# Kernel optimization log

Measured on AMD Instinct MI355X. Metric: run time of the kernel, lower is better.

Reference implementation:

```python
import jax, jax.numpy as jnp
import numpy as np

C = 1024   # hidden_size
H = 16     # num_heads
D = C // H # head dim
M = 4096   # mlp hidden
T = 1024   # motion seq len
B = 8      # batch
TA = 1024  # audio seq len


def _w(key, shape):
    return jax.random.normal(key, shape, dtype=jnp.float32) * 0.02


def setup_inputs() -> dict:
    key = jax.random.key(0)
    ks = jax.random.split(key, 32)
    inp = {
        'x': jax.random.normal(ks[0], (T, B, C), dtype=jnp.float32),
        'c': jax.random.normal(ks[1], (B, C), dtype=jnp.float32),
        'padding_mask': jax.random.randint(ks[2], (B, T), 0, 2, dtype=jnp.int32),
        'audio_seq': jax.random.normal(ks[3], (TA, B, C), dtype=jnp.float32),
        'audio_mask': jax.random.randint(ks[4], (B, TA), 0, 2, dtype=jnp.int32),
        # adaLN modulation: SiLU -> Linear(C, 6C)
        'w_ada': _w(ks[5], (C, 6 * C)), 'b_ada': jnp.zeros((6 * C,), jnp.float32),
        # self-attention q/k/v/proj
        'wq': _w(ks[6], (C, C)), 'bq': jnp.zeros((C,), jnp.float32),
        'wk': _w(ks[7], (C, C)), 'bk': jnp.zeros((C,), jnp.float32),
        'wv': _w(ks[8], (C, C)), 'bv': jnp.zeros((C,), jnp.float32),
        'wo': _w(ks[9], (C, C)), 'bo': jnp.zeros((C,), jnp.float32),
        # cross-attention q/k/v/proj
        'cwq': _w(ks[10], (C, C)), 'cbq': jnp.zeros((C,), jnp.float32),
        'cwk': _w(ks[11], (C, C)), 'cbk': jnp.zeros((C,), jnp.float32),
        'cwv': _w(ks[12], (C, C)), 'cbv': jnp.zeros((C,), jnp.float32),
        'cwo': _w(ks[13], (C, C)), 'cbo': jnp.zeros((C,), jnp.float32),
        # MLP fc1/fc2
        'w1': _w(ks[14], (C, M)), 'b1': jnp.zeros((M,), jnp.float32),
        'w2': _w(ks[15], (M, C)), 'b2': jnp.zeros((C,), jnp.float32),
    }
    return inp


def _ln(x):
    # LayerNorm(elementwise_affine=False, eps=1e-6)
    mu = jnp.mean(x, axis=-1, keepdims=True)
    var = jnp.var(x, axis=-1, keepdims=True)
    return (x - mu) * jax.lax.rsqrt(var + 1e-6)


def _modulate(x, shift, scale):
    # batch-first x [B, T, C]; shift/scale [B, C]
    return x * (1.0 + scale[:, None, :]) + shift[:, None, :]


def _mha(xq, xkv, wq, bq, wk, bk, wv, bv, wo, bo, mask):
    # xq [B, Tq, C], xkv [B, Tk, C], mask [B, Tk] (nonzero = masked)
    b, tq, _ = xq.shape
    tk = xkv.shape[1]
    q = (xq @ wq + bq).reshape(b, tq, H, D)
    k = (xkv @ wk + bk).reshape(b, tk, H, D)
    v = (xkv @ wv + bv).reshape(b, tk, H, D)
    att = jnp.einsum('bqhd,bkhd->bhqk', q, k) * (1.0 / np.sqrt(D))
    att = jnp.where(mask[:, None, None, :] != 0, -jnp.inf, att)
    att = jax.nn.softmax(att, axis=-1)
    y = jnp.einsum('bhqk,bkhd->bqhd', att, v).reshape(b, tq, C)
    return y @ wo + bo


def _gelu_tanh(x):
    return jax.nn.gelu(x, approximate=True)


def reference(x, c, padding_mask, audio_seq, audio_mask,
              w_ada, b_ada, wq, bq, wk, bk, wv, bv, wo, bo,
              cwq, cbq, cwk, cbk, cwv, cbv, cwo, cbo,
              w1, b1, w2, b2):
    # adaLN modulation parameters
    mod = jax.nn.silu(c) @ w_ada + b_ada                 # [B, 6C]
    (shift_msa, scale_msa, gate_msa,
     shift_mlp, scale_mlp, gate_mlp) = jnp.split(mod, 6, axis=1)

    # x is sequence-first [T, B, C] (padding_mask batch dim matches x dim 1)
    x_batch = jnp.transpose(x, (1, 0, 2))                # [B, T, C]
    x_mod = _modulate(_ln(x_batch), shift_msa, scale_msa)
    attn_out = _mha(x_mod, x_mod, wq, bq, wk, bk, wv, bv, wo, bo, padding_mask)
    x = x + gate_msa[None, :, :] * jnp.transpose(attn_out, (1, 0, 2))

    # cross attention (reuses msa shift/scale/gate, as in the source)
    xb = jnp.transpose(x, (1, 0, 2))                     # [B, T, C]
    ab = jnp.transpose(audio_seq, (1, 0, 2))             # [B, TA, C]
    x_cross_in = _modulate(_ln(xb), shift_msa, scale_msa)
    cross_out = _mha(x_cross_in, ab, cwq, cbq, cwk, cbk, cwv, cbv, cwo, cbo,
                     audio_mask)
    x = x + gate_msa[None, :, :] * jnp.transpose(cross_out, (1, 0, 2))

    # MLP
    xb = jnp.transpose(x, (1, 0, 2))
    h = _modulate(_ln(xb), shift_mlp, scale_mlp)
    mlp_out = _gelu_tanh(h @ w1 + b1) @ w2 + b2
    x = x + gate_mlp[None, :, :] * jnp.transpose(mlp_out, (1, 0, 2))
    return x
```

## Files before the change

### kernel.cpp

```cpp
#include <hip/hip_runtime.h>
#include <math.h>

#define T_SEQ 1024
#define TA_SEQ 1024
#define BATCH 8
#define CH 1024
#define NH 16
#define HD 64
#define MH 4096

typedef unsigned short u16;
typedef unsigned short u16x4 __attribute__((ext_vector_type(4)));
typedef unsigned short u16x8 __attribute__((ext_vector_type(8)));
typedef __bf16 bf16x8 __attribute__((ext_vector_type(8)));
typedef float f32x4 __attribute__((ext_vector_type(4)));

__device__ __forceinline__ u16 f2bf(float f) {
  unsigned int u = __builtin_bit_cast(unsigned int, f);
  u += 0x7FFFu + ((u >> 16) & 1u);
  return (u16)(u >> 16);
}
__device__ __forceinline__ u16 f2bf_trunc(float f) {
  return (u16)(__builtin_bit_cast(unsigned int, f) >> 16);
}
__device__ __forceinline__ bf16x8 ldbf8(const u16* p) {
  return __builtin_bit_cast(bf16x8, *reinterpret_cast<const u16x8*>(p));
}
__device__ __forceinline__ void gload_lds16(const u16* g, u16* l) {
  __builtin_amdgcn_global_load_lds(
      (const __attribute__((address_space(1))) unsigned int*)g,
      (__attribute__((address_space(3))) unsigned int*)l, 16, 0, 0);
}

#define ASM_BAR()   asm volatile("s_barrier" ::: "memory")
#define ASM_VM8()   asm volatile("s_waitcnt vmcnt(8)" ::: "memory")
#define ASM_VM6()   asm volatile("s_waitcnt vmcnt(6)" ::: "memory")
#define ASM_VM4()   asm volatile("s_waitcnt vmcnt(4)" ::: "memory")
#define ASM_VM3()   asm volatile("s_waitcnt vmcnt(3)" ::: "memory")
#define ASM_VM0()   asm volatile("s_waitcnt vmcnt(0)" ::: "memory")
#define ASM_LGKM0() asm volatile("s_waitcnt lgkmcnt(0)" ::: "memory")

__global__ void k_transpose_w(const float* __restrict__ in, u16* __restrict__ out,
                              int K, int N) {
  __shared__ float tile[32][33];
  int n0 = blockIdx.x * 32, k0 = blockIdx.y * 32;
  int tx = threadIdx.x, ty = threadIdx.y;
#pragma unroll
  for (int i = 0; i < 4; i++)
    tile[ty + i * 8][tx] = in[(size_t)(k0 + ty + i * 8) * N + n0 + tx];
  __syncthreads();
#pragma unroll
  for (int i = 0; i < 4; i++)
    out[(size_t)(n0 + ty + i * 8) * K + k0 + tx] = f2bf(tile[tx][ty + i * 8]);
}

struct P8f { const float* p[8]; };
struct P8u { u16* p[8]; };
__global__ void k_transpose8(P8f in8, P8u out8) {
  const float* __restrict__ in = in8.p[blockIdx.z];
  u16* __restrict__ out = out8.p[blockIdx.z];
  __shared__ float tile[32][33];
  int n0 = blockIdx.x * 32, k0 = blockIdx.y * 32;
  int tx = threadIdx.x, ty = threadIdx.y;
#pragma unroll
  for (int i = 0; i < 4; i++)
    tile[ty + i * 8][tx] = in[(size_t)(k0 + ty + i * 8) * CH + n0 + tx];
  __syncthreads();
#pragma unroll
  for (int i = 0; i < 4; i++)
    out[(size_t)(n0 + ty + i * 8) * CH + k0 + tx] = f2bf(tile[tx][ty + i * 8]);
}

__global__ void k_ada(const float* __restrict__ c, const float* __restrict__ w_ada,
                      const float* __restrict__ b_ada, float* __restrict__ mod) {
  __shared__ float sc[CH];
  int b = blockIdx.y;
  int tid = threadIdx.x;
  for (int i = tid; i < CH; i += 256) {
    float cv = c[b * CH + i];
    sc[i] = cv / (1.0f + expf(-cv));
  }
  __syncthreads();
  int n = blockIdx.x * 256 + tid;
  float acc = 0.0f;
  for (int k = 0; k < CH; k++) acc += sc[k] * w_ada[(size_t)k * (6 * CH) + n];
  mod[(size_t)b * (6 * CH) + n] = acc + b_ada[n];
}

__global__ void k_tbc_to_btc_bf16(const float* __restrict__ in, u16* __restrict__ out) {
  size_t i = (size_t)blockIdx.x * 256 + threadIdx.x;
  int c = (int)(i & (CH - 1));
  size_t tb = i >> 10;
  int b = (int)(tb & (BATCH - 1));
  size_t t = tb >> 3;
  out[((size_t)b * TA_SEQ + t) * CH + c] = f2bf(in[i]);
}

template <int IN_TBC>
__global__ void k_ln_mod(const float* __restrict__ src, const float* __restrict__ mod,
                         u16* __restrict__ out, float* __restrict__ xb_out,
                         int shift_sel, int scale_sel) {
  int row = blockIdx.x;
  int b = row >> 10;
  int tid = threadIdx.x;
  const float* xr;
  if (IN_TBC) {
    int t = row & (T_SEQ - 1);
    xr = src + ((size_t)t * BATCH + b) * CH;
  } else {
    xr = src + (size_t)row * CH;
  }
  float4 v = reinterpret_cast<const float4*>(xr)[tid];
  float s = v.x + v.y + v.z + v.w;
  float s2 = v.x * v.x + v.y * v.y + v.z * v.z + v.w * v.w;
#pragma unroll
  for (int off = 32; off > 0; off >>= 1) {
    s += __shfl_down(s, off);
    s2 += __shfl_down(s2, off);
  }
  __shared__ float red[8];
  __shared__ float stats[2];
  int wid = tid >> 6;
  if ((tid & 63) == 0) { red[wid] = s; red[4 + wid] = s2; }
  __syncthreads();
  if (tid == 0) {
    float a = red[0] + red[1] + red[2] + red[3];
    float a2 = red[4] + red[5] + red[6] + red[7];
    float mu = a * (1.0f / CH);
    float var = a2 * (1.0f / CH) - mu * mu;
    stats[0] = mu;
    stats[1] = rsqrtf(var + 1e-6f);
  }
  __syncthreads();
  float mu = stats[0], rs = stats[1];
  int c0 = tid * 4;
  if (IN_TBC)
    reinterpret_cast<float4*>(xb_out + (size_t)row * CH)[tid] = v;
  const float* sh = mod + (size_t)b * (6 * CH) + (size_t)shift_sel * CH + c0;
  const float* scl = mod + (size_t)b * (6 * CH) + (size_t)scale_sel * CH + c0;
  float xs[4] = {v.x, v.y, v.z, v.w};
  u16x4 o;
#pragma unroll
  for (int j = 0; j < 4; j++)
    o[j] = f2bf((xs[j] - mu) * rs * (1.0f + scl[j]) + sh[j]);
  *reinterpret_cast<u16x4*>(out + (size_t)row * CH + c0) = o;
}

__device__ __forceinline__ void mfma_quad(const bf16x8 (&af)[4], const bf16x8 (&bfr)[4],
                                          f32x4 (*arow)[4]) {
#pragma unroll
  for (int mi = 0; mi < 4; mi++)
#pragma unroll
    for (int ni = 0; ni < 4; ni++)
      arow[mi][ni] = __builtin_amdgcn_mfma_f32_16x16x32_bf16(af[mi], bfr[ni],
                                                             arow[mi][ni], 0, 0, 0);
}

__device__ __forceinline__ void gemm256_core(
    const u16* __restrict__ A, const u16* __restrict__ Bt, int K,
    int m0, int n0, int tid, u16* AS, u16* BS, f32x4 (&acc)[8][4]) {
  int wid = tid >> 6, lane = tid & 63;
  int wr = wid >> 2, wc = wid & 3;
  int lrow = lane & 15, quad = lane >> 4;
  int sx = (quad ^ ((lrow >> 1) & 3)) * 8;
  int aRow = wr * 128 + lrow;
  int bRow = wc * 64 + lrow;
  int rA = tid >> 2;
  int qsw = (((tid & 3) ^ ((tid >> 3) & 3)) << 3);
  const u16* gA = A + (size_t)(m0 + rA) * K + qsw;
  const u16* gB = Bt + (size_t)(n0 + rA) * K + qsw;
  const size_t r128 = (size_t)128 * K;
  u16* dA = AS + tid * 8;
  u16* dB = BS + tid * 8;
  const int NT = K >> 6;

#define STGA(dd, hh, tt) do { const u16* s_ = gA + ((tt) * 64 + (hh) * 32); \
    u16* d_ = dA + ((dd) * 2 + (hh)) * 8192; \
    gload_lds16(s_, d_); gload_lds16(s_ + r128, d_ + 4096); } while (0)
#define STGB(dd, hh, tt) do { const u16* s_ = gB + ((tt) * 64 + (hh) * 32); \
    u16* d_ = dB + ((dd) * 2 + (hh)) * 8192; \
    gload_lds16(s_, d_); gload_lds16(s_ + r128, d_ + 4096); } while (0)
#define RD_A(dd, kk, mh) do { const u16* b_ = AS + ((dd) * 2 + (kk)) * 8192; \
    int r_ = aRow + (mh) * 64; \
    af[0] = ldbf8(&b_[(r_) * 32 + sx]); \
    af[1] = ldbf8(&b_[(r_ + 16) * 32 + sx]); \
    af[2] = ldbf8(&b_[(r_ + 32) * 32 + sx]); \
    af[3] = ldbf8(&b_[(r_ + 48) * 32 + sx]); } while (0)
#define RD_B(dd, kk) do { const u16* b_ = BS + ((dd) * 2 + (kk)) * 8192; \
    bfr[0] = ldbf8(&b_[(bRow) * 32 + sx]); \
    bfr[1] = ldbf8(&b_[(bRow + 16) * 32 + sx]); \
    bfr[2] = ldbf8(&b_[(bRow + 32) * 32 + sx]); \
    bfr[3] = ldbf8(&b_[(bRow + 48) * 32 + sx]); } while (0)
#define PHASE_TAIL(mh) do { ASM_LGKM0(); __builtin_amdgcn_sched_barrier(0); \
    __builtin_amdgcn_s_setprio(1); mfma_quad(af, bfr, acc + (mh) * 4); \
    __builtin_amdgcn_s_setprio(0); ASM_BAR(); } while (0)

  STGA(0, 0, 0); STGB(0, 0, 0); STGA(0, 1, 0); STGB(0, 1, 0);
  STGA(1, 0, 1); STGB(1, 0, 1);
  ASM_VM8(); ASM_BAR();

  bf16x8 af[4], bfr[4];
  for (int t = 0; t < NT; ++t) {
    int d = t & 1;
    RD_A(d, 0, 0); RD_B(d, 0);
    if (t + 1 < NT) STGA(d ^ 1, 1, t + 1);
    PHASE_TAIL(0);
    RD_A(d, 0, 1);
    if (t + 1 < NT) STGB(d ^ 1, 1, t + 1);
    if (t == NT - 1) { ASM_VM0(); } else { ASM_VM8(); }
    PHASE_TAIL(1);
    RD_A(d, 1, 0); RD_B(d, 1);
    if (t + 2 < NT) STGA(d, 0, t + 2);
    PHASE_TAIL(0);
    RD_A(d, 1, 1);
    if (t + 2 < NT) STGB(d, 0, t + 2);
    if (t < NT - 2) { ASM_VM8(); } else if (t == NT - 2) { ASM_VM4(); }
    PHASE_TAIL(1);
  }
#undef STGA
#undef STGB
#undef RD_A
#undef RD_B
#undef PHASE_TAIL
}

template <int EPI>
__global__ __launch_bounds__(512, 2) void k_gemm256(
    const u16* __restrict__ A, const u16* __restrict__ Bt,
    const float* __restrict__ bias, u16* __restrict__ out_bf,
    float* __restrict__ xb, const float* __restrict__ mod, int gate_sel,
    int M, int N, int K) {
  __shared__ u16 AS[2 * 2 * 8192];
  __shared__ u16 BS[2 * 2 * 8192];
  int m0 = blockIdx.x * 256, n0 = blockIdx.y * 256;
  int tid = threadIdx.x;
  int wid = tid >> 6, lane = tid & 63;
  int wr = wid >> 2, wc = wid & 3;
  int lrow = lane & 15, quad = lane >> 4;
  f32x4 acc[8][4];
#pragma unroll
  for (int mi = 0; mi < 8; mi++)
#pragma unroll
    for (int ni = 0; ni < 4; ni++) acc[mi][ni] = {0.f, 0.f, 0.f, 0.f};
  gemm256_core(A, Bt, K, m0, n0, tid, AS, BS, acc);
#pragma unroll
  for (int mi = 0; mi < 8; mi++)
#pragma unroll
    for (int ni = 0; ni < 4; ni++) {
      int col = n0 + wc * 64 + ni * 16 + lrow;
      float bval = bias[col];
#pragma unroll
      for (int r = 0; r < 4; r++) {
        int row = m0 + wr * 128 + mi * 16 + quad * 4 + r;
        float v = acc[mi][ni][r] + bval;
        if (EPI == 1) {
          int b = row >> 10;
          float g = mod[(size_t)b * (6 * CH) + (size_t)gate_sel * CH + col];
          xb[(size_t)row * N + col] += g * v;
        } else if (EPI == 2) {
          float t2 = 2.3021181302f * (v + 0.044715f * v * v * v);
          float gel = v * __builtin_amdgcn_rcpf(1.0f + exp2f(-t2));
          out_bf[(size_t)row * N + col] = f2bf(gel);
        } else {
          out_bf[(size_t)row * N + col] = f2bf(v * 0.18033688011112042f);
        }
      }
    }
}

__global__ __launch_bounds__(512, 2) void k_qkv256(
    const u16* __restrict__ A, const u16* __restrict__ Bt,
    const float* __restrict__ bq, const float* __restrict__ bk,
    const float* __restrict__ bv,
    u16* __restrict__ qout, u16* __restrict__ kout, u16* __restrict__ vt) {
  __shared__ u16 AS[2 * 2 * 8192];
  __shared__ u16 BS[2 * 2 * 8192];
  int m0 = blockIdx.x * 256, n0 = blockIdx.y * 256;
  int tid = threadIdx.x;
  int wid = tid >> 6, lane = tid & 63;
  int wr = wid >> 2, wc = wid & 3;
  int lrow = lane & 15, quad = lane >> 4;
  f32x4 acc[8][4];
#pragma unroll
  for (int mi = 0; mi < 8; mi++)
#pragma unroll
    for (int ni = 0; ni < 4; ni++) acc[mi][ni] = {0.f, 0.f, 0.f, 0.f};
  gemm256_core(A, Bt, CH, m0, n0, tid, AS, BS, acc);
  int seg = n0 >> 10;
  const float* bias = (seg == 0) ? bq : (seg == 1) ? bk : bv;
#pragma unroll
  for (int mi = 0; mi < 8; mi++)
#pragma unroll
    for (int ni = 0; ni < 4; ni++) {
      int col = (n0 & 1023) + wc * 64 + ni * 16 + lrow;
      float bval = bias[col];
      int row0 = m0 + wr * 128 + mi * 16 + quad * 4;
      if (seg == 0) {
#pragma unroll
        for (int r = 0; r < 4; r++)
          qout[(size_t)(row0 + r) * CH + col] =
              f2bf((acc[mi][ni][r] + bval) * 0.18033688011112042f);
      } else if (seg == 1) {
#pragma unroll
        for (int r = 0; r < 4; r++)
          kout[(size_t)(row0 + r) * CH + col] = f2bf(acc[mi][ni][r] + bval);
      } else {
        u16x4 pk;
#pragma unroll
        for (int r = 0; r < 4; r++) pk[r] = f2bf(acc[mi][ni][r] + bval);
        int b = row0 >> 10, t0 = row0 & 1023;
        int h = col >> 6, d = col & 63;
        *reinterpret_cast<u16x4*>(
            vt + (((size_t)(b * NH + h) * HD + d) << 10) + t0) = pk;
      }
    }
}

__global__ __launch_bounds__(512, 2) void k_kv256(
    const u16* __restrict__ A, const u16* __restrict__ Bt,
    const float* __restrict__ bk, const float* __restrict__ bv,
    u16* __restrict__ kout, u16* __restrict__ vt) {
  __shared__ u16 AS[2 * 2 * 8192];
  __shared__ u16 BS[2 * 2 * 8192];
  int m0 = blockIdx.x * 256, n0 = blockIdx.y * 256;
  int tid = threadIdx.x;
  int wid = tid >> 6, lane = tid & 63;
  int wr = wid >> 2, wc = wid & 3;
  int lrow = lane & 15, quad = lane >> 4;
  f32x4 acc[8][4];
#pragma unroll
  for (int mi = 0; mi < 8; mi++)
#pragma unroll
    for (int ni = 0; ni < 4; ni++) acc[mi][ni] = {0.f, 0.f, 0.f, 0.f};
  gemm256_core(A, Bt, CH, m0, n0, tid, AS, BS, acc);
  int seg = n0 >> 10;
  const float* bias = (seg == 0) ? bk : bv;
#pragma unroll
  for (int mi = 0; mi < 8; mi++)
#pragma unroll
    for (int ni = 0; ni < 4; ni++) {
      int col = (n0 & 1023) + wc * 64 + ni * 16 + lrow;
      float bval = bias[col];
      int row0 = m0 + wr * 128 + mi * 16 + quad * 4;
      if (seg == 0) {
#pragma unroll
        for (int r = 0; r < 4; r++)
          kout[(size_t)(row0 + r) * CH + col] = f2bf(acc[mi][ni][r] + bval);
      } else {
        u16x4 pk;
#pragma unroll
        for (int r = 0; r < 4; r++) pk[r] = f2bf(acc[mi][ni][r] + bval);
        int b = row0 >> 10, t0 = row0 & 1023;
        int h = col >> 6, d = col & 63;
        *reinterpret_cast<u16x4*>(
            vt + (((size_t)(b * NH + h) * HD + d) << 10) + t0) = pk;
      }
    }
}

__device__ __forceinline__ void mfma_duo(const bf16x8 (&af)[4], const bf16x8 (&bfr)[2],
                                         f32x4 (*arow)[2]) {
#pragma unroll
  for (int mi = 0; mi < 4; mi++)
#pragma unroll
    for (int ni = 0; ni < 2; ni++)
      arow[mi][ni] = __builtin_amdgcn_mfma_f32_16x16x32_bf16(af[mi], bfr[ni],
                                                             arow[mi][ni], 0, 0, 0);
}

__device__ __forceinline__ void gemm128n_core(
    const u16* __restrict__ A, const u16* __restrict__ Bt, int K,
    int m0, int n0, int tid, u16* AS, u16* BS, f32x4 (&acc)[8][2]) {
  int wid = tid >> 6, lane = tid & 63;
  int wr = wid >> 2, wc = wid & 3;
  int lrow = lane & 15, quad = lane >> 4;
  int sx = (quad ^ ((lrow >> 1) & 3)) * 8;
  int aRow = wr * 128 + lrow;
  int bRow = wc * 32 + lrow;
  int rA = tid >> 2;
  int qsw = (((tid & 3) ^ ((tid >> 3) & 3)) << 3);
  const u16* gA = A + (size_t)(m0 + rA) * K + qsw;
  const u16* gB = Bt + (size_t)(n0 + rA) * K + qsw;
  const size_t r128 = (size_t)128 * K;
  u16* dA = AS + tid * 8;
  u16* dB = BS + tid * 8;
  const int NT = K >> 6;

#define STGA(dd, hh, tt) do { const u16* s_ = gA + ((tt) * 64 + (hh) * 32); \
    u16* d_ = dA + ((dd) * 2 + (hh)) * 8192; \
    gload_lds16(s_, d_); gload_lds16(s_ + r128, d_ + 4096); } while (0)
#define STGB(dd, hh, tt) do { const u16* s_ = gB + ((tt) * 64 + (hh) * 32); \
    u16* d_ = dB + ((dd) * 2 + (hh)) * 4096; \
    gload_lds16(s_, d_); } while (0)
#define RD_A(dd, kk, mh) do { const u16* b_ = AS + ((dd) * 2 + (kk)) * 8192; \
    int r_ = aRow + (mh) * 64; \
    af[0] = ldbf8(&b_[(r_) * 32 + sx]); \
    af[1] = ldbf8(&b_[(r_ + 16) * 32 + sx]); \
    af[2] = ldbf8(&b_[(r_ + 32) * 32 + sx]); \
    af[3] = ldbf8(&b_[(r_ + 48) * 32 + sx]); } while (0)
#define RD_B(dd, kk) do { const u16* b_ = BS + ((dd) * 2 + (kk)) * 4096; \
    bfr[0] = ldbf8(&b_[(bRow) * 32 + sx]); \
    bfr[1] = ldbf8(&b_[(bRow + 16) * 32 + sx]); } while (0)
#define PHASE_TAIL(mh) do { ASM_LGKM0(); __builtin_amdgcn_sched_barrier(0); \
    __builtin_amdgcn_s_setprio(1); mfma_duo(af, bfr, acc + (mh) * 4); \
    __builtin_amdgcn_s_setprio(0); ASM_BAR(); } while (0)

  STGA(0, 0, 0); STGB(0, 0, 0); STGA(0, 1, 0); STGB(0, 1, 0);
  STGA(1, 0, 1); STGB(1, 0, 1);
  ASM_VM6(); ASM_BAR();

  bf16x8 af[4], bfr[2];
  for (int t = 0; t < NT; ++t) {
    int d = t & 1;
    RD_A(d, 0, 0); RD_B(d, 0);
    if (t + 1 < NT) STGA(d ^ 1, 1, t + 1);
    PHASE_TAIL(0);
    RD_A(d, 0, 1);
    if (t + 1 < NT) STGB(d ^ 1, 1, t + 1);
    if (t == NT - 1) { ASM_VM0(); } else { ASM_VM6(); }
    PHASE_TAIL(1);
    RD_A(d, 1, 0); RD_B(d, 1);
    if (t + 2 < NT) STGA(d, 0, t + 2);
    PHASE_TAIL(0);
    RD_A(d, 1, 1);
    if (t + 2 < NT) STGB(d, 0, t + 2);
    if (t < NT - 2) { ASM_VM6(); } else if (t == NT - 2) { ASM_VM3(); }
    PHASE_TAIL(1);
  }
#undef STGA
#undef STGB
#undef RD_A
#undef RD_B
#undef PHASE_TAIL
}

template <int EPI>
__global__ __launch_bounds__(512, 2) void k_gemm128n(
    const u16* __restrict__ A, const u16* __restrict__ Bt,
    const float* __restrict__ bias, u16* __restrict__ out_bf,
    float* __restrict__ xb, float* __restrict__ dout,
    const float* __restrict__ mod, int gate_sel, int M, int N, int K) {
  __shared__ u16 AS[2 * 2 * 8192];
  __shared__ u16 BS[2 * 2 * 4096];
  int m0 = blockIdx.x * 256, n0 = blockIdx.y * 128;
  int tid = threadIdx.x;
  int wid = tid >> 6, lane = tid & 63;
  int wr = wid >> 2, wc = wid & 3;
  int lrow = lane & 15, quad = lane >> 4;
  f32x4 acc[8][2];
#pragma unroll
  for (int mi = 0; mi < 8; mi++)
#pragma unroll
    for (int ni = 0; ni < 2; ni++) acc[mi][ni] = {0.f, 0.f, 0.f, 0.f};
  gemm128n_core(A, Bt, K, m0, n0, tid, AS, BS, acc);
#pragma unroll
  for (int mi = 0; mi < 8; mi++)
#pragma unroll
    for (int ni = 0; ni < 2; ni++) {
      int col = n0 + wc * 32 + ni * 16 + lrow;
      float bval = bias[col];
#pragma unroll
      for (int r = 0; r < 4; r++) {
        int row = m0 + wr * 128 + mi * 16 + quad * 4 + r;
        float v = acc[mi][ni][r] + bval;
        if (EPI == 1) {
          int b = row >> 10;
          float g = mod[(size_t)b * (6 * CH) + (size_t)gate_sel * CH + col];
          xb[(size_t)row * N + col] += g * v;
        } else if (EPI == 3) {
          out_bf[(size_t)row * N + col] = f2bf(v * 0.18033688011112042f);
        } else {
          int b = row >> 10, t = row & (T_SEQ - 1);
          float g = mod[(size_t)b * (6 * CH) + (size_t)gate_sel * CH + col];
          dout[((size_t)t * BATCH + b) * CH + col] =
              xb[(size_t)row * N + col] + g * v;
        }
      }
    }
}

__global__ __launch_bounds__(256, 2) void k_attn(
    const u16* __restrict__ Q, const u16* __restrict__ Kb,
    const u16* __restrict__ vt, const int* __restrict__ mask,
    u16* __restrict__ Y) {
  int qt = blockIdx.x, h = blockIdx.y, b = blockIdx.z;
  int tid = threadIdx.x, wid = tid >> 6, lane = tid & 63;
  int lrow = lane & 15, quad = lane >> 4;
  int qbase = qt * 256 + wid * 64;

  __shared__ u16 P[4][4][16][72];

  bf16x8 aq[4][2];
#pragma unroll
  for (int st = 0; st < 4; st++) {
    size_t qoff = ((size_t)(b * T_SEQ + qbase + st * 16 + lrow)) * CH + h * HD;
    aq[st][0] = ldbf8(Q + qoff + quad * 8);
    aq[st][1] = ldbf8(Q + qoff + 32 + quad * 8);
  }

  u16x8 uo;
#pragma unroll
  for (int j = 0; j < 8; j++) uo[j] = (lrow == 0) ? (u16)0x3F80 : (u16)0;
  bf16x8 ones = __builtin_bit_cast(bf16x8, uo);

  const int* mrow = mask + (size_t)b * T_SEQ;
  const u16* ksrc = Kb + ((size_t)(b * T_SEQ) + lrow) * CH + h * HD + quad * 8;
  const u16* vsrc = vt + (((size_t)(b * NH + h) * HD + lrow) << 10) + quad * 8;

  f32x4 o[4][5];
#pragma unroll
  for (int st = 0; st < 4; st++)
#pragma unroll
    for (int dc = 0; dc < 5; dc++) o[st][dc] = {0.f, 0.f, 0.f, 0.f};

  for (int kt = 0; kt < 16; kt++) {
    int kb = kt * 64;
    bf16x8 kf[8];
    float mb[4];
#pragma unroll
    for (int sub = 0; sub < 4; sub++) {
      const u16* kp = ksrc + (size_t)(kb + sub * 16) * CH;
      kf[sub * 2] = ldbf8(kp);
      kf[sub * 2 + 1] = ldbf8(kp + 32);
      mb[sub] = mrow[kb + sub * 16 + lrow] ? -INFINITY : 0.0f;
    }
    bf16x8 vf[8];
#pragma unroll
    for (int dc = 0; dc < 4; dc++) {
      const u16* vp = vsrc + (size_t)(dc * 16) * 1024 + kb;
      vf[dc * 2] = ldbf8(vp);
      vf[dc * 2 + 1] = ldbf8(vp + 32);
    }
#pragma unroll
    for (int st = 0; st < 4; st++) {
#pragma unroll
      for (int sub = 0; sub < 4; sub++) {
        f32x4 z = {0.f, 0.f, 0.f, 0.f};
        z = __builtin_amdgcn_mfma_f32_16x16x32_bf16(aq[st][0], kf[sub * 2], z, 0, 0, 0);
        z = __builtin_amdgcn_mfma_f32_16x16x32_bf16(aq[st][1], kf[sub * 2 + 1], z, 0, 0, 0);
        float mbv = mb[sub];
#pragma unroll
        for (int r = 0; r < 4; r++) {
          float p = exp2f(z[r] + mbv);
          P[wid][st][quad * 4 + r][sub * 16 + lrow] = f2bf_trunc(p);
        }
      }
    }
#pragma unroll
    for (int st = 0; st < 4; st++) {
      bf16x8 pf0 = ldbf8(&P[wid][st][lrow][quad * 8]);
      bf16x8 pf1 = ldbf8(&P[wid][st][lrow][32 + quad * 8]);
#pragma unroll
      for (int dc = 0; dc < 4; dc++) {
        o[st][dc] = __builtin_amdgcn_mfma_f32_16x16x32_bf16(pf0, vf[dc * 2], o[st][dc], 0, 0, 0);
        o[st][dc] = __builtin_amdgcn_mfma_f32_16x16x32_bf16(pf1, vf[dc * 2 + 1], o[st][dc], 0, 0, 0);
      }
      o[st][4] = __builtin_amdgcn_mfma_f32_16x16x32_bf16(pf0, ones, o[st][4], 0, 0, 0);
      o[st][4] = __builtin_amdgcn_mfma_f32_16x16x32_bf16(pf1, ones, o[st][4], 0, 0, 0);
    }
  }

#pragma unroll
  for (int st = 0; st < 4; st++)
#pragma unroll
    for (int r = 0; r < 4; r++) {
      float l = __shfl(o[st][4][r], lane & 48);
      float linv = 1.0f / l;
      int qr = qbase + st * 16 + quad * 4 + r;
      size_t yo = ((size_t)(b * T_SEQ + qr)) * CH + h * HD;
#pragma unroll
      for (int dc = 0; dc < 4; dc++)
        Y[yo + dc * 16 + lrow] = f2bf(o[st][dc][r] * linv);
    }
}

extern "C" void kernel_launch(void* const* d_in, const int* in_sizes, int n_in,
                              void* d_out, int out_size, void* d_ws, size_t ws_size,
                              hipStream_t stream) {
  const float* x     = (const float*)d_in[0];
  const float* c     = (const float*)d_in[1];
  const int*   pmask = (const int*)d_in[2];
  const float* audio = (const float*)d_in[3];
  const int*   amask = (const int*)d_in[4];
  const float* w_ada = (const float*)d_in[5];
  const float* b_ada = (const float*)d_in[6];
  const float* wq = (const float*)d_in[7];  const float* bq = (const float*)d_in[8];
  const float* wk = (const float*)d_in[9];  const float* bk = (const float*)d_in[10];
  const float* wv = (const float*)d_in[11]; const float* bv = (const float*)d_in[12];
  const float* wo = (const float*)d_in[13]; const float* bo = (const float*)d_in[14];
  const float* cwq = (const float*)d_in[15]; const float* cbq = (const float*)d_in[16];
  const float* cwk = (const float*)d_in[17]; const float* cbk = (const float*)d_in[18];
  const float* cwv = (const float*)d_in[19]; const float* cbv = (const float*)d_in[20];
  const float* cwo = (const float*)d_in[21]; const float* cbo = (const float*)d_in[22];
  const float* w1 = (const float*)d_in[23]; const float* b1 = (const float*)d_in[24];
  const float* w2 = (const float*)d_in[25]; const float* b2 = (const float*)d_in[26];

  char* wsb = (char*)d_ws;
  size_t off = 0;
  auto alloc = [&](size_t bytes) {
    char* p = wsb + off;
    off += (bytes + 255) & ~(size_t)255;
    return p;
  };
  const size_t SQ = (size_t)CH * CH * 2;
  u16* wqT  = (u16*)alloc(SQ);
  u16* wkT  = (u16*)alloc(SQ);
  u16* wvT  = (u16*)alloc(SQ);
  u16* woT  = (u16*)alloc(SQ);
  u16* cwqT = (u16*)alloc(SQ);
  u16* cwkT = (u16*)alloc(SQ);
  u16* cwvT = (u16*)alloc(SQ);
  u16* cwoT = (u16*)alloc(SQ);
  u16* w1T  = (u16*)alloc((size_t)CH * MH * 2);
  u16* w2T  = (u16*)alloc((size_t)CH * MH * 2);
  float* mod = (float*)alloc((size_t)BATCH * 6 * CH * 4);
  float* xb  = (float*)alloc((size_t)BATCH * T_SEQ * CH * 4);
  u16* xm    = (u16*)alloc((size_t)BATCH * T_SEQ * CH * 2);
  u16* hbuf  = (u16*)alloc((size_t)BATCH * T_SEQ * MH * 2);
  u16* qbuf  = hbuf;
  u16* kbuf  = hbuf + (size_t)BATCH * T_SEQ * CH;
  u16* ybuf  = hbuf + (size_t)2 * BATCH * T_SEQ * CH;
  u16* vt    = hbuf + (size_t)3 * BATCH * T_SEQ * CH;
  u16* abuf  = (u16*)alloc((size_t)BATCH * TA_SEQ * CH * 2);
  (void)ws_size; (void)in_sizes; (void)n_in; (void)out_size;

  const int NE = T_SEQ * BATCH * CH;
  dim3 tb32(32, 8);

  P8f src8; P8u dst8;
  src8.p[0] = wq;  dst8.p[0] = wqT;
  src8.p[1] = wk;  dst8.p[1] = wkT;
  src8.p[2] = wv;  dst8.p[2] = wvT;
  src8.p[3] = wo;  dst8.p[3] = woT;
  src8.p[4] = cwq; dst8.p[4] = cwqT;
  src8.p[5] = cwk; dst8.p[5] = cwkT;
  src8.p[6] = cwv; dst8.p[6] = cwvT;
  src8.p[7] = cwo; dst8.p[7] = cwoT;
  k_transpose8<<<dim3(CH / 32, CH / 32, 8), tb32, 0, stream>>>(src8, dst8);
  k_transpose_w<<<dim3(MH / 32, CH / 32), tb32, 0, stream>>>(w1, w1T, CH, MH);
  k_transpose_w<<<dim3(CH / 32, MH / 32), tb32, 0, stream>>>(w2, w2T, MH, CH);

  k_ada<<<dim3(6 * CH / 256, BATCH), 256, 0, stream>>>(c, w_ada, b_ada, mod);
  k_tbc_to_btc_bf16<<<NE / 256, 256, 0, stream>>>(audio, abuf);

  k_ln_mod<1><<<BATCH * T_SEQ, 256, 0, stream>>>(x, mod, xm, xb, 0, 1);
  k_qkv256<<<dim3(32, 12), 512, 0, stream>>>(xm, wqT, bq, bk, bv, qbuf, kbuf, vt);
  k_attn<<<dim3(T_SEQ / 256, NH, BATCH), 256, 0, stream>>>(qbuf, kbuf, vt, pmask, ybuf);
  k_gemm128n<1><<<dim3(32, 8), 512, 0, stream>>>(ybuf, woT, bo, nullptr, xb, nullptr, mod, 2, 8192, CH, CH);

  k_ln_mod<0><<<BATCH * T_SEQ, 256, 0, stream>>>(xb, mod, xm, nullptr, 0, 1);
  k_gemm128n<3><<<dim3(32, 8), 512, 0, stream>>>(xm, cwqT, cbq, qbuf, nullptr, nullptr, nullptr, 0, 8192, CH, CH);
  k_kv256<<<dim3(32, 8), 512, 0, stream>>>(abuf, cwkT, cbk, cbv, kbuf, vt);
  k_attn<<<dim3(T_SEQ / 256, NH, BATCH), 256, 0, stream>>>(qbuf, kbuf, vt, amask, ybuf);
  k_gemm128n<1><<<dim3(32, 8), 512, 0, stream>>>(ybuf, cwoT, cbo, nullptr, xb, nullptr, mod, 2, 8192, CH, CH);

  k_ln_mod<0><<<BATCH * T_SEQ, 256, 0, stream>>>(xb, mod, xm, nullptr, 3, 4);
  k_gemm256<2><<<dim3(32, 16), 512, 0, stream>>>(xm, w1T, b1, hbuf, nullptr, nullptr, 0, 8192, MH, CH);
  k_gemm128n<4><<<dim3(32, 8), 512, 0, stream>>>(hbuf, w2T, b2, nullptr, xb, (float*)d_out, mod, 5, 8192, CH, MH);
}
```

Baseline: 840.8 us.

## Restructure GEMM main loop into triple-buffered full-K-tile pipeline with fewer barriers

```diff
diff --git a/kernel.cpp b/kernel.cpp
--- a/kernel.cpp
+++ b/kernel.cpp
@@ -36,7 +36,6 @@
 #define ASM_VM8()   asm volatile("s_waitcnt vmcnt(8)" ::: "memory")
 #define ASM_VM6()   asm volatile("s_waitcnt vmcnt(6)" ::: "memory")
 #define ASM_VM4()   asm volatile("s_waitcnt vmcnt(4)" ::: "memory")
-#define ASM_VM3()   asm volatile("s_waitcnt vmcnt(3)" ::: "memory")
 #define ASM_VM0()   asm volatile("s_waitcnt vmcnt(0)" ::: "memory")
 #define ASM_LGKM0() asm volatile("s_waitcnt lgkmcnt(0)" ::: "memory")
 
@@ -386,52 +385,66 @@
   u16* dB = BS + tid * 8;
   const int NT = K >> 6;
 
-#define STGA(dd, hh, tt) do { const u16* s_ = gA + ((tt) * 64 + (hh) * 32); \
-    u16* d_ = dA + ((dd) * 2 + (hh)) * 8192; \
-    gload_lds16(s_, d_); gload_lds16(s_ + r128, d_ + 4096); } while (0)
-#define STGB(dd, hh, tt) do { const u16* s_ = gB + ((tt) * 64 + (hh) * 32); \
-    u16* d_ = dB + ((dd) * 2 + (hh)) * 4096; \
-    gload_lds16(s_, d_); } while (0)
-#define RD_A(dd, kk, mh) do { const u16* b_ = AS + ((dd) * 2 + (kk)) * 8192; \
+#define STG(bb, tt) do { \
+    const u16* sa_ = gA + (size_t)(tt) * 64; \
+    u16* da_ = dA + (bb) * 16384; \
+    gload_lds16(sa_, da_); \
+    gload_lds16(sa_ + r128, da_ + 4096); \
+    gload_lds16(sa_ + 32, da_ + 8192); \
+    gload_lds16(sa_ + 32 + r128, da_ + 12288); \
+    const u16* sb_ = gB + (size_t)(tt) * 64; \
+    u16* db_ = dB + (bb) * 8192; \
+    gload_lds16(sb_, db_); \
+    gload_lds16(sb_ + 32, db_ + 4096); } while (0)
+#define RD_A8(bb, mh) do { \
+    const u16* a0_ = AS + (bb) * 16384; \
     int r_ = aRow + (mh) * 64; \
-    af[0] = ldbf8(&b_[(r_) * 32 + sx]); \
-    af[1] = ldbf8(&b_[(r_ + 16) * 32 + sx]); \
-    af[2] = ldbf8(&b_[(r_ + 32) * 32 + sx]); \
-    af[3] = ldbf8(&b_[(r_ + 48) * 32 + sx]); } while (0)
-#define RD_B(dd, kk) do { const u16* b_ = BS + ((dd) * 2 + (kk)) * 4096; \
-    bfr[0] = ldbf8(&b_[(bRow) * 32 + sx]); \
-    bfr[1] = ldbf8(&b_[(bRow + 16) * 32 + sx]); } while (0)
-#define PHASE_TAIL(mh) do { ASM_LGKM0(); __builtin_amdgcn_sched_barrier(0); \
-    __builtin_amdgcn_s_setprio(1); mfma_duo(af, bfr, acc + (mh) * 4); \
-    __builtin_amdgcn_s_setprio(0); ASM_BAR(); } while (0)
-
-  STGA(0, 0, 0); STGB(0, 0, 0); STGA(0, 1, 0); STGB(0, 1, 0);
-  STGA(1, 0, 1); STGB(1, 0, 1);
+    af0[0] = ldbf8(&a0_[(r_) * 32 + sx]); \
+    af0[1] = ldbf8(&a0_[(r_ + 16) * 32 + sx]); \
+    af0[2] = ldbf8(&a0_[(r_ + 32) * 32 + sx]); \
+    af0[3] = ldbf8(&a0_[(r_ + 48) * 32 + sx]); \
+    const u16* a1_ = a0_ + 8192; \
+    af1[0] = ldbf8(&a1_[(r_) * 32 + sx]); \
+    af1[1] = ldbf8(&a1_[(r_ + 16) * 32 + sx]); \
+    af1[2] = ldbf8(&a1_[(r_ + 32) * 32 + sx]); \
+    af1[3] = ldbf8(&a1_[(r_ + 48) * 32 + sx]); } while (0)
+#define RD_B4(bb) do { \
+    const u16* b0_ = BS + (bb) * 8192; \
+    bf0[0] = ldbf8(&b0_[(bRow) * 32 + sx]); \
+    bf0[1] = ldbf8(&b0_[(bRow + 16) * 32 + sx]); \
+    const u16* b1_ = b0_ + 4096; \
+    bf1[0] = ldbf8(&b1_[(bRow) * 32 + sx]); \
+    bf1[1] = ldbf8(&b1_[(bRow + 16) * 32 + sx]); } while (0)
+
+  STG(0, 0);
+  STG(1, 1);
   ASM_VM6(); ASM_BAR();
 
-  bf16x8 af[4], bfr[2];
+  bf16x8 af0[4], af1[4], bf0[2], bf1[2];
+  int bi = 0;
   for (int t = 0; t < NT; ++t) {
-    int d = t & 1;
-    RD_A(d, 0, 0); RD_B(d, 0);
-    if (t + 1 < NT) STGA(d ^ 1, 1, t + 1);
-    PHASE_TAIL(0);
-    RD_A(d, 0, 1);
-    if (t + 1 < NT) STGB(d ^ 1, 1, t + 1);
-    if (t == NT - 1) { ASM_VM0(); } else { ASM_VM6(); }
-    PHASE_TAIL(1);
-    RD_A(d, 1, 0); RD_B(d, 1);
-    if (t + 2 < NT) STGA(d, 0, t + 2);
-    PHASE_TAIL(0);
-    RD_A(d, 1, 1);
-    if (t + 2 < NT) STGB(d, 0, t + 2);
-    if (t < NT - 2) { ASM_VM6(); } else if (t == NT - 2) { ASM_VM3(); }
-    PHASE_TAIL(1);
-  }
-#undef STGA
-#undef STGB
-#undef RD_A
-#undef RD_B
-#undef PHASE_TAIL
+    int bs = bi + 2; if (bs >= 3) bs -= 3;
+    RD_A8(bi, 0); RD_B4(bi);
+    if (t + 2 < NT) STG(bs, t + 2);
+    ASM_LGKM0(); __builtin_amdgcn_sched_barrier(0);
+    __builtin_amdgcn_s_setprio(1);
+    mfma_duo(af0, bf0, acc + 0);
+    mfma_duo(af1, bf1, acc + 0);
+    __builtin_amdgcn_s_setprio(0);
+    ASM_BAR();
+    RD_A8(bi, 1);
+    if (t < NT - 2) { ASM_VM6(); } else if (t == NT - 2) { ASM_VM0(); }
+    ASM_LGKM0(); __builtin_amdgcn_sched_barrier(0);
+    __builtin_amdgcn_s_setprio(1);
+    mfma_duo(af0, bf0, acc + 4);
+    mfma_duo(af1, bf1, acc + 4);
+    __builtin_amdgcn_s_setprio(0);
+    ASM_BAR();
+    bi = (bi == 2) ? 0 : bi + 1;
+  }
+#undef STG
+#undef RD_A8
+#undef RD_B4
 }
 
 template <int EPI>
@@ -440,8 +453,8 @@
     const float* __restrict__ bias, u16* __restrict__ out_bf,
     float* __restrict__ xb, float* __restrict__ dout,
     const float* __restrict__ mod, int gate_sel, int M, int N, int K) {
-  __shared__ u16 AS[2 * 2 * 8192];
-  __shared__ u16 BS[2 * 2 * 4096];
+  __shared__ u16 AS[3 * 16384];
+  __shared__ u16 BS[3 * 8192];
   int m0 = blockIdx.x * 256, n0 = blockIdx.y * 128;
   int tid = threadIdx.x;
   int wid = tid >> 6, lane = tid & 63;
```

Result: slower. 911.6 us (+8.4%).
